# Optimization experiments

Hardware: AMD Instinct MI355X
Metric: run time of the kernel (lower is better)

## Reference

```python
import jax, jax.numpy as jnp
import numpy as np

B, C, T = 4, 1024, 2048
H = 16            # num_heads
G = 32            # GroupNorm groups (normalization(channels) == GroupNorm(32, C))
EPS = 1e-5


def setup_inputs() -> dict:
    key = jax.random.key(0)
    ks = jax.random.split(key, 7)
    x = jax.random.normal(ks[0], (B, C, T), dtype=jnp.float32)
    gn_scale = jax.random.normal(ks[1], (C,), dtype=jnp.float32) * 0.02 + 1.0
    gn_bias = jax.random.normal(ks[2], (C,), dtype=jnp.float32) * 0.02
    qkv_w = jax.random.normal(ks[3], (3 * C, C), dtype=jnp.float32) / np.sqrt(C)
    qkv_b = jax.random.normal(ks[4], (3 * C,), dtype=jnp.float32) * 0.02
    # NOTE: original zero-inits proj_out; randomized here so output != x for testing.
    proj_w = jax.random.normal(ks[5], (C, C), dtype=jnp.float32) / np.sqrt(C)
    proj_b = jax.random.normal(ks[6], (C,), dtype=jnp.float32) * 0.02
    return {"x": x, "gn_scale": gn_scale, "gn_bias": gn_bias,
            "qkv_w": qkv_w, "qkv_b": qkv_b, "proj_w": proj_w, "proj_b": proj_b}


def reference(x, gn_scale, gn_bias, qkv_w, qkv_b, proj_w, proj_b):
    b, c, t = x.shape
    ch = c // H
    # GroupNorm(32, C) over (channels-in-group, T)
    xg = x.reshape(b, G, c // G, t)
    mean = xg.mean(axis=(2, 3), keepdims=True)
    var = xg.var(axis=(2, 3), keepdims=True)
    xn = ((xg - mean) * jax.lax.rsqrt(var + EPS)).reshape(b, c, t)
    xn = xn * gn_scale[None, :, None] + gn_bias[None, :, None]
    # 1x1 conv QKV: [B, 3C, T]
    qkv = jnp.einsum('oc,bct->bot', qkv_w, xn) + qkv_b[None, :, None]
    q, k, v = jnp.split(qkv, 3, axis=1)
    # split heads -> [B*H, ch, T]
    q = q.reshape(b * H, ch, t)
    k = k.reshape(b * H, ch, t)
    v = v.reshape(b * H, ch, t)
    scale = 1.0 / np.sqrt(np.sqrt(ch)).astype(np.float32)
    # full T x T attention weights, softmax in fp32 (as original)
    w = jnp.einsum('bct,bcs->bts', q * scale, k * scale)
    w = jax.nn.softmax(w.astype(jnp.float32), axis=-1).astype(w.dtype)
    a = jnp.einsum('bts,bcs->bct', w, v).reshape(b, c, t)
    # 1x1 conv projection + residual
    h = jnp.einsum('oc,bct->bot', proj_w, a) + proj_b[None, :, None]
    return x + h
```

## Files before the change

kernel.cpp:

```cpp
#include <hip/hip_runtime.h>
#include <hip/hip_bf16.h>
#include <stdint.h>

#define Bn 4
#define Cn 1024
#define Tn 2048
#define Hn 16
#define Gn 32
#define SCALE_Q 0.18033688f

typedef short short8  __attribute__((ext_vector_type(8)));
typedef short short4_t __attribute__((ext_vector_type(4)));
typedef float float4_t __attribute__((ext_vector_type(4)));
typedef unsigned int uint2_t __attribute__((ext_vector_type(2)));

__device__ __forceinline__ short f2bf(float f) {
    uint32_t u = __float_as_uint(f);
    uint32_t r = (u + 0x7FFFu + ((u >> 16) & 1u)) >> 16;
    return (short)r;
}

__device__ __forceinline__ float exp2_fast(float x) {
#if __has_builtin(__builtin_amdgcn_exp2f)
    return __builtin_amdgcn_exp2f(x);
#else
    return exp2f(x);
#endif
}

__device__ __forceinline__ uint32_t pack_bf16_trunc(float lo, float hi) {
#if __has_builtin(__builtin_amdgcn_perm)
    return __builtin_amdgcn_perm(__float_as_uint(hi), __float_as_uint(lo), 0x07060302u);
#else
    return (__float_as_uint(lo) >> 16) | (__float_as_uint(hi) & 0xFFFF0000u);
#endif
}

__device__ __forceinline__ void permswap32(uint32_t& x, uint32_t& y) {
#if __has_builtin(__builtin_amdgcn_permlane32_swap)
    uint2_t r = __builtin_amdgcn_permlane32_swap(x, y, false, false);
    x = r[0]; y = r[1];
#else
    asm volatile("v_permlane32_swap_b32 %0, %1" : "+v"(x), "+v"(y));
#endif
}
__device__ __forceinline__ void permswap16(uint32_t& x, uint32_t& y) {
#if __has_builtin(__builtin_amdgcn_permlane16_swap)
    uint2_t r = __builtin_amdgcn_permlane16_swap(x, y, false, false);
    x = r[0]; y = r[1];
#else
    asm volatile("v_permlane16_swap_b32 %0, %1" : "+v"(x), "+v"(y));
#endif
}

#define GLL16(gptr, lptr)                                                      \
    __builtin_amdgcn_global_load_lds(                                          \
        (const __attribute__((address_space(1))) unsigned int*)(gptr),         \
        (__attribute__((address_space(3))) unsigned int*)(lptr), 16, 0, 0)

__global__ __launch_bounds__(256) void cvt_w(const float* __restrict__ src,
                                             short* __restrict__ dst, int n4) {
    int i = blockIdx.x * 256 + threadIdx.x;
    if (i < n4) {
        float4_t v = reinterpret_cast<const float4_t*>(src)[i];
        short4_t o;
        o[0] = f2bf(v[0]); o[1] = f2bf(v[1]); o[2] = f2bf(v[2]); o[3] = f2bf(v[3]);
        reinterpret_cast<short4_t*>(dst)[i] = o;
    }
}

__global__ __launch_bounds__(256) void groupnorm_k(const float* __restrict__ x,
                                                   const float* __restrict__ gs,
                                                   const float* __restrict__ gb,
                                                   short* __restrict__ xnT) {
    int blk = blockIdx.x;
    int b = blk >> 5, g = blk & 31;
    const float* base = x + ((size_t)(b * Cn + g * 32)) * Tn;
    int tid = threadIdx.x;

    float s = 0.f, ss = 0.f;
    const float4_t* b4 = reinterpret_cast<const float4_t*>(base);
    for (int i = tid; i < 16384; i += 256) {
        float4_t v = b4[i];
        s  += v[0] + v[1] + v[2] + v[3];
        ss += v[0]*v[0] + v[1]*v[1] + v[2]*v[2] + v[3]*v[3];
    }
    #pragma unroll
    for (int m = 1; m < 64; m <<= 1) { s += __shfl_xor(s, m); ss += __shfl_xor(ss, m); }
    __shared__ float red[8];
    int wave = tid >> 6;
    if ((tid & 63) == 0) { red[wave * 2] = s; red[wave * 2 + 1] = ss; }
    __syncthreads();
    float ts  = red[0] + red[2] + red[4] + red[6];
    float tss = red[1] + red[3] + red[5] + red[7];
    float mean = ts * (1.f / 65536.f);
    float var  = tss * (1.f / 65536.f) - mean * mean;
    float rstd = rsqrtf(var + 1e-5f);

    __shared__ float tile[64][33];
    for (int t0 = 0; t0 < Tn; t0 += 64) {
        #pragma unroll
        for (int k = 0; k < 8; k++) {
            int e = tid + k * 256;
            int c = e >> 6, tt = e & 63;
            float v = base[c * Tn + t0 + tt];
            tile[tt][c] = (v - mean) * rstd * gs[g * 32 + c] + gb[g * 32 + c];
        }
        __syncthreads();
        #pragma unroll
        for (int k = 0; k < 8; k++) {
            int f = tid + k * 256;
            int tt = f >> 5, c = f & 31;
            xnT[((size_t)(b * Tn + t0 + tt)) * Cn + g * 32 + c] = f2bf(tile[tt][c]);
        }
        __syncthreads();
    }
}

template <int MODE>
__global__ __launch_bounds__(256) void gemm_k(const short* __restrict__ W,
                                              const short* __restrict__ Bm,
                                              const float* __restrict__ bias,
                                              const float* __restrict__ xres,
                                              short* __restrict__ qkT,
                                              short* __restrict__ vbuf,
                                              float* __restrict__ outp) {
    constexpr int K = 1024;
    constexpr int NT = K / 64;
    __shared__ short As[2][128 * 64];
    __shared__ short Bs[2][128 * 64];

    int m0 = blockIdx.x * 128, n0 = blockIdx.y * 128, b = blockIdx.z;
    int tid = threadIdx.x;
    int wave = tid >> 6, lane = tid & 63, quad = lane >> 4, l15 = lane & 15;
    int wm = wave >> 1, wn = wave & 1;
    const short* Ab = W + (size_t)m0 * K;
    const short* Bb = Bm + ((size_t)b * Tn + n0) * K;

    float4_t acc[4][4];
    float4_t z = {0.f, 0.f, 0.f, 0.f};
    #pragma unroll
    for (int i = 0; i < 4; i++)
        #pragma unroll
        for (int j = 0; j < 4; j++) acc[i][j] = z;

    int sw = l15 & 7;

    auto stage = [&](int buf, int k0) {
        #pragma unroll
        for (int r = 0; r < 4; r++) {
            int cid = r * 256 + tid;
            int row = cid >> 3, j = cid & 7;
            int ch = j ^ (row & 7);
            GLL16(Ab + (size_t)row * K + k0 + ch * 8, &As[buf][cid * 8]);
            GLL16(Bb + (size_t)row * K + k0 + ch * 8, &Bs[buf][cid * 8]);
        }
    };

    stage(0, 0);
    stage(1, 64);
    __builtin_amdgcn_sched_barrier(0);
    asm volatile("s_waitcnt vmcnt(8)" ::: "memory");
    __builtin_amdgcn_sched_barrier(0);
    __builtin_amdgcn_s_barrier();
    __builtin_amdgcn_sched_barrier(0);

    for (int it = 0; it < NT; ++it) {
        int cur = it & 1;
        #pragma unroll
        for (int kk = 0; kk < 2; kk++) {
            short8 af[4], bfg[4];
            #pragma unroll
            for (int mi = 0; mi < 4; mi++)
                af[mi] = *reinterpret_cast<const short8*>(
                    &As[cur][(wm * 64 + mi * 16 + l15) * 64 + ((4 * kk + quad) ^ sw) * 8]);
            #pragma unroll
            for (int ni = 0; ni < 4; ni++)
                bfg[ni] = *reinterpret_cast<const short8*>(
                    &Bs[cur][(wn * 64 + ni * 16 + l15) * 64 + ((4 * kk + quad) ^ sw) * 8]);
            #pragma unroll
            for (int mi = 0; mi < 4; mi++)
                #pragma unroll
                for (int ni = 0; ni < 4; ni++)
                    acc[mi][ni] = __builtin_amdgcn_mfma_f32_16x16x32_bf16(
                        af[mi], bfg[ni], acc[mi][ni], 0, 0, 0);
        }
        __builtin_amdgcn_sched_barrier(0);
        __builtin_amdgcn_s_barrier();
        __builtin_amdgcn_sched_barrier(0);
        if (it + 2 < NT) stage(cur, (it + 2) * 64);
        __builtin_amdgcn_sched_barrier(0);
        if (it + 2 < NT) {
            asm volatile("s_waitcnt vmcnt(8)" ::: "memory");
        } else if (it + 1 < NT) {
            asm volatile("s_waitcnt vmcnt(0)" ::: "memory");
        }
        __builtin_amdgcn_sched_barrier(0);
        __builtin_amdgcn_s_barrier();
        __builtin_amdgcn_sched_barrier(0);
    }

    if (MODE == 0) {
        #pragma unroll
        for (int mi = 0; mi < 4; mi++) {
            int mrow = m0 + wm * 64 + mi * 16 + quad * 4;
            #pragma unroll
            for (int ni = 0; ni < 4; ni++) {
                int t = n0 + wn * 64 + ni * 16 + l15;
                if (mrow < 2048) {
                    int hh = mrow >> 6, ch = mrow & 63;
                    float sc = (mrow < 1024) ? SCALE_Q : 1.0f;
                    short4_t pk;
                    #pragma unroll
                    for (int r = 0; r < 4; r++)
                        pk[r] = f2bf((acc[mi][ni][r] + bias[mrow + r]) * sc);
                    *reinterpret_cast<short4_t*>(
                        &qkT[(((size_t)b * 32 + hh) * Tn + t) * 64 + ch]) = pk;
                } else {
                    int c = mrow - 2048;
                    #pragma unroll
                    for (int r = 0; r < 4; r++)
                        vbuf[((size_t)b * Cn + c + r) * Tn + t] =
                            f2bf(acc[mi][ni][r] + bias[mrow + r]);
                }
            }
        }
    } else {
        #pragma unroll
        for (int mi = 0; mi < 4; mi++) {
            int mrow = m0 + wm * 64 + mi * 16 + quad * 4;
            #pragma unroll
            for (int ni = 0; ni < 4; ni++) {
                int t = n0 + wn * 64 + ni * 16 + l15;
                #pragma unroll
                for (int r = 0; r < 4; r++) {
                    size_t idx = ((size_t)b * Cn + mrow + r) * Tn + t;
                    outp[idx] = xres[idx] + bias[mrow + r] + acc[mi][ni][r];
                }
            }
        }
    }
}

__global__ __launch_bounds__(512, 4) void attn_k(const short* __restrict__ qkT,
                                                 const short* __restrict__ vbuf,
                                                 short* __restrict__ aT) {
    __shared__ short ks[2][64 * 72];
    __shared__ short vs[2][64 * 72];
    int bh = blockIdx.y; int b = bh >> 4, h = bh & 15;
    int t0 = blockIdx.x * 256;
    int tid = threadIdx.x;
    int wave = tid >> 6, lane = tid & 63, quad = lane >> 4, l15 = lane & 15;
    const short* qb = qkT + (((size_t)b * 32 + h) * Tn) * 64;
    const short* kb = qkT + (((size_t)b * 32 + 16 + h) * Tn) * 64;
    const short* vb = vbuf + ((size_t)b * Cn + h * 64) * Tn;
    int tw = t0 + wave * 32;

    short8 qf[2][2];
    #pragma unroll
    for (int tni = 0; tni < 2; tni++)
        #pragma unroll
        for (int kk = 0; kk < 2; kk++)
            qf[tni][kk] = *reinterpret_cast<const short8*>(
                qb + ((size_t)(tw + tni * 16 + l15)) * 64 + kk * 32 + quad * 8);

    short8 ones;
    #pragma unroll
    for (int i = 0; i < 8; i++) ones[i] = (short)0x3F80;

    float4_t z = {0.f, 0.f, 0.f, 0.f};
    float4_t acc[2][4], lacc[2];
    #pragma unroll
    for (int i = 0; i < 2; i++) {
        lacc[i] = z;
        #pragma unroll
        for (int j = 0; j < 4; j++) acc[i][j] = z;
    }

    int srow = tid >> 3, soff = (tid & 7) * 8;
    const short* kgp = kb + (size_t)srow * 64 + soff;
    const short* vgp = vb + (size_t)srow * Tn + soff;
    short* krd = &ks[0][0]; short* kwr = &ks[1][0];
    short* vrd = &vs[0][0]; short* vwr = &vs[1][0];
    int sdst = srow * 72 + soff;

    {
        uint4 k0v = *reinterpret_cast<const uint4*>(kgp);
        uint4 v0v = *reinterpret_cast<const uint4*>(vgp);
        *reinterpret_cast<uint4*>(&krd[sdst]) = k0v;
        *reinterpret_cast<uint4*>(&vrd[sdst]) = v0v;
    }
    __syncthreads();

    for (int it = 0; it < Tn / 64; ++it) {
        uint4 knx, vnx;
        if (it < Tn / 64 - 1) {
            knx = *reinterpret_cast<const uint4*>(kgp + (size_t)(it + 1) * 64 * 64);
            vnx = *reinterpret_cast<const uint4*>(vgp + (size_t)(it + 1) * 64);
        }

        #pragma unroll
        for (int pr = 0; pr < 2; pr++) {
            uint32_t pk[2][2][2];
            #pragma unroll
            for (int half = 0; half < 2; half++) {
                int smi = pr * 2 + half;
                float4_t sa[2] = {z, z};
                __builtin_amdgcn_s_setprio(1);
                #pragma unroll
                for (int kk = 0; kk < 2; kk++) {
                    short8 kf = *reinterpret_cast<const short8*>(
                        &krd[(smi * 16 + l15) * 72 + kk * 32 + quad * 8]);
                    #pragma unroll
                    for (int tni = 0; tni < 2; tni++)
                        sa[tni] = __builtin_amdgcn_mfma_f32_16x16x32_bf16(
                            kf, qf[tni][kk], sa[tni], 0, 0, 0);
                }
                __builtin_amdgcn_s_setprio(0);
                #pragma unroll
                for (int tni = 0; tni < 2; tni++) {
                    float p0 = exp2_fast(sa[tni][0]);
                    float p1 = exp2_fast(sa[tni][1]);
                    float p2 = exp2_fast(sa[tni][2]);
                    float p3 = exp2_fast(sa[tni][3]);
                    pk[half][tni][0] = pack_bf16_trunc(p0, p1);
                    pk[half][tni][1] = pack_bf16_trunc(p2, p3);
                }
            }
            short8 vf[4];
            #pragma unroll
            for (int ci = 0; ci < 4; ci++)
                vf[ci] = *reinterpret_cast<const short8*>(
                    &vrd[(ci * 16 + l15) * 72 + pr * 32 + quad * 8]);
            #pragma unroll
            for (int tni = 0; tni < 2; tni++) {
                uint32_t x0 = pk[0][tni][0], y0 = pk[1][tni][0];
                permswap32(x0, y0); permswap16(x0, y0);
                uint32_t x1 = pk[0][tni][1], y1 = pk[1][tni][1];
                permswap32(x1, y1); permswap16(x1, y1);
                uint4 afu = {x0, x1, y0, y1};
                short8 af = *reinterpret_cast<short8*>(&afu);
                __builtin_amdgcn_s_setprio(1);
                lacc[tni] = __builtin_amdgcn_mfma_f32_16x16x32_bf16(
                    af, ones, lacc[tni], 0, 0, 0);
                #pragma unroll
                for (int ci = 0; ci < 4; ci++)
                    acc[tni][ci] = __builtin_amdgcn_mfma_f32_16x16x32_bf16(
                        af, vf[ci], acc[tni][ci], 0, 0, 0);
                __builtin_amdgcn_s_setprio(0);
            }
        }

        if (it < Tn / 64 - 1) {
            *reinterpret_cast<uint4*>(&kwr[sdst]) = knx;
            *reinterpret_cast<uint4*>(&vwr[sdst]) = vnx;
        }
        __syncthreads();
        short* tk = krd; krd = kwr; kwr = tk;
        short* tv = vrd; vrd = vwr; vwr = tv;
    }

    #pragma unroll
    for (int tni = 0; tni < 2; tni++) {
        #pragma unroll
        for (int r = 0; r < 4; r++) {
            float rl = 1.0f / lacc[tni][r];
            int t = tw + tni * 16 + quad * 4 + r;
            #pragma unroll
            for (int ci = 0; ci < 4; ci++) {
                int ch = ci * 16 + l15;
                aT[((size_t)b * Tn + t) * Cn + h * 64 + ch] =
                    f2bf(acc[tni][ci][r] * rl);
            }
        }
    }
}

extern "C" void kernel_launch(void* const* d_in, const int* in_sizes, int n_in,
                              void* d_out, int out_size, void* d_ws, size_t ws_size,
                              hipStream_t stream) {
    const float* x     = (const float*)d_in[0];
    const float* gs    = (const float*)d_in[1];
    const float* gb    = (const float*)d_in[2];
    const float* qkvw  = (const float*)d_in[3];
    const float* qkvb  = (const float*)d_in[4];
    const float* projw = (const float*)d_in[5];
    const float* projb = (const float*)d_in[6];
    float* out = (float*)d_out;

    char* ws = (char*)d_ws;
    short* wqkv  = (short*)(ws + 0);
    short* wproj = (short*)(ws + 6291456);
    short* xnT   = (short*)(ws + 8388608);
    short* aT    = (short*)(ws + 8388608);
    short* qkT   = (short*)(ws + 25165824);
    short* vbuf  = (short*)(ws + 58720256);

    cvt_w<<<dim3(3072), dim3(256), 0, stream>>>(qkvw, wqkv, 786432);
    cvt_w<<<dim3(1024), dim3(256), 0, stream>>>(projw, wproj, 262144);
    groupnorm_k<<<dim3(Bn * Gn), dim3(256), 0, stream>>>(x, gs, gb, xnT);
    gemm_k<0><<<dim3(24, 16, 4), dim3(256), 0, stream>>>(wqkv, xnT, qkvb, nullptr,
                                                         qkT, vbuf, nullptr);
    attn_k<<<dim3(8, 64), dim3(512), 0, stream>>>(qkT, vbuf, aT);
    gemm_k<1><<<dim3(8, 16, 4), dim3(256), 0, stream>>>(wproj, aT, projb, x,
                                                        nullptr, nullptr, out);
}
```

Baseline: 311.2 us.

## Stage attention K/V tiles via direct global-to-LDS loads with XOR swizzle

Replaces the register-staged double buffer in the attention kernel with direct global-to-LDS loads (GLL16), prefetching two tiles ahead and synchronising with explicit vmcnt waits and s_barrier. The padded 72-stride LDS layout is replaced by an unpadded 64-stride layout with XOR swizzling to avoid bank conflicts. Odd and even waves also process the two PV halves in opposite order to spread LDS access. This aims to free VGPRs and hide global load latency, at the cost of two barriers per iteration and reliance on correct vmcnt accounting.

```diff
diff --git a/kernel.cpp b/kernel.cpp
--- a/kernel.cpp
+++ b/kernel.cpp
@@ -245,8 +245,9 @@
 __global__ __launch_bounds__(512, 4) void attn_k(const short* __restrict__ qkT,
                                                  const short* __restrict__ vbuf,
                                                  short* __restrict__ aT) {
-    __shared__ short ks[2][64 * 72];
-    __shared__ short vs[2][64 * 72];
+    constexpr int NT = Tn / 64;
+    __shared__ short ks[2][64 * 64];
+    __shared__ short vs[2][64 * 64];
     int bh = blockIdx.y; int b = bh >> 4, h = bh & 15;
     int t0 = blockIdx.x * 256;
     int tid = threadIdx.x;
@@ -255,6 +256,7 @@
     const short* kb = qkT + (((size_t)b * 32 + 16 + h) * Tn) * 64;
     const short* vb = vbuf + ((size_t)b * Cn + h * 64) * Tn;
     int tw = t0 + wave * 32;
+    int rsw = l15 & 7;
 
     short8 qf[2][2];
     #pragma unroll
@@ -277,30 +279,31 @@
         for (int j = 0; j < 4; j++) acc[i][j] = z;
     }
 
-    int srow = tid >> 3, soff = (tid & 7) * 8;
-    const short* kgp = kb + (size_t)srow * 64 + soff;
-    const short* vgp = vb + (size_t)srow * Tn + soff;
-    short* krd = &ks[0][0]; short* kwr = &ks[1][0];
-    short* vrd = &vs[0][0]; short* vwr = &vs[1][0];
-    int sdst = srow * 72 + soff;
-
-    {
-        uint4 k0v = *reinterpret_cast<const uint4*>(kgp);
-        uint4 v0v = *reinterpret_cast<const uint4*>(vgp);
-        *reinterpret_cast<uint4*>(&krd[sdst]) = k0v;
-        *reinterpret_cast<uint4*>(&vrd[sdst]) = v0v;
-    }
-    __syncthreads();
-
-    for (int it = 0; it < Tn / 64; ++it) {
-        uint4 knx, vnx;
-        if (it < Tn / 64 - 1) {
-            knx = *reinterpret_cast<const uint4*>(kgp + (size_t)(it + 1) * 64 * 64);
-            vnx = *reinterpret_cast<const uint4*>(vgp + (size_t)(it + 1) * 64);
-        }
-
-        #pragma unroll
-        for (int pr = 0; pr < 2; pr++) {
+    int srow = tid >> 3, sj = tid & 7;
+    int ssw = (sj ^ (srow & 7)) * 8;
+    const short* kgp = kb + (size_t)srow * 64 + ssw;
+    const short* vgp = vb + (size_t)srow * Tn + ssw;
+
+    auto stageKV = [&](int buf, int t) {
+        GLL16(kgp + (size_t)t * 4096, &ks[buf][tid * 8]);
+        GLL16(vgp + (size_t)t * 64,   &vs[buf][tid * 8]);
+    };
+
+    stageKV(0, 0);
+    stageKV(1, 1);
+    __builtin_amdgcn_sched_barrier(0);
+    asm volatile("s_waitcnt vmcnt(2)" ::: "memory");
+    __builtin_amdgcn_sched_barrier(0);
+    __builtin_amdgcn_s_barrier();
+    __builtin_amdgcn_sched_barrier(0);
+
+    int prs = wave & 1;
+
+    for (int it = 0; it < NT; ++it) {
+        int cur = it & 1;
+        #pragma unroll
+        for (int p2 = 0; p2 < 2; p2++) {
+            int pr = p2 ^ prs;
             uint32_t pk[2][2][2];
             #pragma unroll
             for (int half = 0; half < 2; half++) {
@@ -310,7 +313,7 @@
                 #pragma unroll
                 for (int kk = 0; kk < 2; kk++) {
                     short8 kf = *reinterpret_cast<const short8*>(
-                        &krd[(smi * 16 + l15) * 72 + kk * 32 + quad * 8]);
+                        &ks[cur][(smi * 16 + l15) * 64 + ((kk * 4 + quad) ^ rsw) * 8]);
                     #pragma unroll
                     for (int tni = 0; tni < 2; tni++)
                         sa[tni] = __builtin_amdgcn_mfma_f32_16x16x32_bf16(
@@ -321,17 +324,17 @@
                 for (int tni = 0; tni < 2; tni++) {
                     float p0 = exp2_fast(sa[tni][0]);
                     float p1 = exp2_fast(sa[tni][1]);
-                    float p2 = exp2_fast(sa[tni][2]);
+                    float p2v = exp2_fast(sa[tni][2]);
                     float p3 = exp2_fast(sa[tni][3]);
                     pk[half][tni][0] = pack_bf16_trunc(p0, p1);
-                    pk[half][tni][1] = pack_bf16_trunc(p2, p3);
+                    pk[half][tni][1] = pack_bf16_trunc(p2v, p3);
                 }
             }
             short8 vf[4];
             #pragma unroll
             for (int ci = 0; ci < 4; ci++)
                 vf[ci] = *reinterpret_cast<const short8*>(
-                    &vrd[(ci * 16 + l15) * 72 + pr * 32 + quad * 8]);
+                    &vs[cur][(ci * 16 + l15) * 64 + ((pr * 4 + quad) ^ rsw) * 8]);
             #pragma unroll
             for (int tni = 0; tni < 2; tni++) {
                 uint32_t x0 = pk[0][tni][0], y0 = pk[1][tni][0];
@@ -351,13 +354,19 @@
             }
         }
 
-        if (it < Tn / 64 - 1) {
-            *reinterpret_cast<uint4*>(&kwr[sdst]) = knx;
-            *reinterpret_cast<uint4*>(&vwr[sdst]) = vnx;
-        }
-        __syncthreads();
-        short* tk = krd; krd = kwr; kwr = tk;
-        short* tv = vrd; vrd = vwr; vwr = tv;
+        __builtin_amdgcn_sched_barrier(0);
+        __builtin_amdgcn_s_barrier();
+        __builtin_amdgcn_sched_barrier(0);
+        if (it + 2 < NT) stageKV(cur, it + 2);
+        __builtin_amdgcn_sched_barrier(0);
+        if (it + 2 < NT) {
+            asm volatile("s_waitcnt vmcnt(2)" ::: "memory");
+        } else if (it + 1 < NT) {
+            asm volatile("s_waitcnt vmcnt(0)" ::: "memory");
+        }
+        __builtin_amdgcn_sched_barrier(0);
+        __builtin_amdgcn_s_barrier();
+        __builtin_amdgcn_sched_barrier(0);
     }
 
     #pragma unroll
```

Result: slower. 326.8 us (+5.0%).

## Split GroupNorm into parallel stats and apply kernels, merge weight conversions

Applied to the files above, without the earlier changes.

GroupNorm previously ran as only 128 blocks, each streaming a whole 256 KB group twice. It is now split into a 1024-block partial-statistics kernel and a 1024-block apply kernel, each handling a T-slice, with the partials held in workspace that qkT later overwrites. The two weight-conversion launches are also merged into one kernel. This raises parallelism and drops a launch, at the cost of an extra launch plus a small read of the partial sums.

```diff
diff --git a/kernel.cpp b/kernel.cpp
--- a/kernel.cpp
+++ b/kernel.cpp
@@ -58,30 +58,29 @@
         (const __attribute__((address_space(1))) unsigned int*)(gptr),         \
         (__attribute__((address_space(3))) unsigned int*)(lptr), 16, 0, 0)
 
-__global__ __launch_bounds__(256) void cvt_w(const float* __restrict__ src,
-                                             short* __restrict__ dst, int n4) {
+__global__ __launch_bounds__(256) void cvt_w2(const float* __restrict__ srcA,
+                                              const float* __restrict__ srcB,
+                                              short* __restrict__ dst) {
     int i = blockIdx.x * 256 + threadIdx.x;
-    if (i < n4) {
-        float4_t v = reinterpret_cast<const float4_t*>(src)[i];
-        short4_t o;
-        o[0] = f2bf(v[0]); o[1] = f2bf(v[1]); o[2] = f2bf(v[2]); o[3] = f2bf(v[3]);
-        reinterpret_cast<short4_t*>(dst)[i] = o;
-    }
-}
-
-__global__ __launch_bounds__(256) void groupnorm_k(const float* __restrict__ x,
-                                                   const float* __restrict__ gs,
-                                                   const float* __restrict__ gb,
-                                                   short* __restrict__ xnT) {
-    int blk = blockIdx.x;
-    int b = blk >> 5, g = blk & 31;
-    const float* base = x + ((size_t)(b * Cn + g * 32)) * Tn;
+    float4_t v = (i < 786432)
+        ? reinterpret_cast<const float4_t*>(srcA)[i]
+        : reinterpret_cast<const float4_t*>(srcB)[i - 786432];
+    short4_t o;
+    o[0] = f2bf(v[0]); o[1] = f2bf(v[1]); o[2] = f2bf(v[2]); o[3] = f2bf(v[3]);
+    reinterpret_cast<short4_t*>(dst)[i] = o;
+}
+
+__global__ __launch_bounds__(256) void gn_stats(const float* __restrict__ x,
+                                                float* __restrict__ part) {
+    int lin = blockIdx.x;
+    int sl = lin & 7, g = (lin >> 3) & 31, b = lin >> 8;
+    const float4_t* base = reinterpret_cast<const float4_t*>(
+        x + ((size_t)(b * Cn + g * 32)) * Tn) + sl * 2048;
     int tid = threadIdx.x;
-
     float s = 0.f, ss = 0.f;
-    const float4_t* b4 = reinterpret_cast<const float4_t*>(base);
-    for (int i = tid; i < 16384; i += 256) {
-        float4_t v = b4[i];
+    #pragma unroll
+    for (int k = 0; k < 8; k++) {
+        float4_t v = base[tid + k * 256];
         s  += v[0] + v[1] + v[2] + v[3];
         ss += v[0]*v[0] + v[1]*v[1] + v[2]*v[2] + v[3]*v[3];
     }
@@ -91,14 +90,35 @@
     int wave = tid >> 6;
     if ((tid & 63) == 0) { red[wave * 2] = s; red[wave * 2 + 1] = ss; }
     __syncthreads();
-    float ts  = red[0] + red[2] + red[4] + red[6];
-    float tss = red[1] + red[3] + red[5] + red[7];
+    if (tid == 0) {
+        part[lin * 2]     = red[0] + red[2] + red[4] + red[6];
+        part[lin * 2 + 1] = red[1] + red[3] + red[5] + red[7];
+    }
+}
+
+__global__ __launch_bounds__(256) void gn_apply(const float* __restrict__ x,
+                                                const float* __restrict__ gs,
+                                                const float* __restrict__ gb,
+                                                const float* __restrict__ part,
+                                                short* __restrict__ xnT) {
+    int lin = blockIdx.x;
+    int sl = lin & 7, g = (lin >> 3) & 31, b = lin >> 8;
+    const float* base = x + ((size_t)(b * Cn + g * 32)) * Tn;
+    int tid = threadIdx.x;
+    int pb = (lin >> 3) << 3;
+    float ts = 0.f, tss = 0.f;
+    #pragma unroll
+    for (int i = 0; i < 8; i++) {
+        ts  += part[(pb + i) * 2];
+        tss += part[(pb + i) * 2 + 1];
+    }
     float mean = ts * (1.f / 65536.f);
     float var  = tss * (1.f / 65536.f) - mean * mean;
     float rstd = rsqrtf(var + 1e-5f);
 
     __shared__ float tile[64][33];
-    for (int t0 = 0; t0 < Tn; t0 += 64) {
+    int tbase = sl * 256;
+    for (int t0 = tbase; t0 < tbase + 256; t0 += 64) {
         #pragma unroll
         for (int k = 0; k < 8; k++) {
             int e = tid + k * 256;
@@ -394,11 +414,12 @@
     short* xnT   = (short*)(ws + 8388608);
     short* aT    = (short*)(ws + 8388608);
     short* qkT   = (short*)(ws + 25165824);
+    float* gnp   = (float*)(ws + 25165824);
     short* vbuf  = (short*)(ws + 58720256);
 
-    cvt_w<<<dim3(3072), dim3(256), 0, stream>>>(qkvw, wqkv, 786432);
-    cvt_w<<<dim3(1024), dim3(256), 0, stream>>>(projw, wproj, 262144);
-    groupnorm_k<<<dim3(Bn * Gn), dim3(256), 0, stream>>>(x, gs, gb, xnT);
+    cvt_w2<<<dim3(4096), dim3(256), 0, stream>>>(qkvw, projw, wqkv);
+    gn_stats<<<dim3(1024), dim3(256), 0, stream>>>(x, gnp);
+    gn_apply<<<dim3(1024), dim3(256), 0, stream>>>(x, gs, gb, gnp, xnT);
     gemm_k<0><<<dim3(24, 16, 4), dim3(256), 0, stream>>>(wqkv, xnT, qkvb, nullptr,
                                                          qkT, vbuf, nullptr);
     attn_k<<<dim3(8, 64), dim3(512), 0, stream>>>(qkT, vbuf, aT);
```

New measurement: 272.4 us, median of 2. 12.5% less time.
